# Performance work log

Measured on AMD Instinct MI355X. Metric: run time of the kernel, lower is better.

## Reference

```python
import jax, jax.numpy as jnp
import numpy as np

EPS = 1e-06
K = 4          # hc_mult
D = 2048       # hidden_size
SINKHORN_ITERS = 20


def setup_inputs() -> dict:
    key = jax.random.key(0)
    k1, k2, k3 = jax.random.split(key, 3)
    B, S = 2, 4096
    x = jax.random.normal(k1, (B, S, K, D), dtype=jnp.float32)
    out = jax.random.normal(k2, (B, S, D), dtype=jnp.float32)
    out_dim = (2 + K) * K  # 24
    # matches nn.init.normal_(std=1/sqrt(K*D))
    W = jax.random.normal(k3, (out_dim, K * D), dtype=jnp.float32) / np.sqrt(K * D)
    scale = jnp.ones((3,), dtype=jnp.float32)
    base = jnp.zeros((out_dim,), dtype=jnp.float32)
    return {"x": x, "out": out, "W": W, "scale": scale, "base": base}


def _sinkhorn(m, n_iters=SINKHORN_ITERS, eps=EPS):
    # one priming column normalization, then (n_iters-1) row/col cycles
    m = m / (jnp.sum(m, axis=-2, keepdims=True) + eps)
    for _ in range(max(n_iters - 1, 0)):
        m = m / (jnp.sum(m, axis=-1, keepdims=True) + eps)
        m = m / (jnp.sum(m, axis=-2, keepdims=True) + eps)
    return m


def reference(x, out, W, scale, base):
    out_dtype = x.dtype
    # --- _packed_logits: flatten K streams, RMS-normalize, project (fp32) ---
    flat = x.reshape(*x.shape[:-2], K * D).astype(jnp.float32)      # [B,S,K*D]
    rsqrt = jax.lax.rsqrt(jnp.mean(flat * flat, axis=-1, keepdims=True) + EPS)
    logits = jnp.einsum('bsf,of->bso', flat * rsqrt, W)             # [B,S,24]
    # --- compute_weights: split into pre/post/comb ---
    pre_logit = logits[..., :K] * scale[0] + base[:K]
    post_logit = logits[..., K:2 * K] * scale[1] + base[K:2 * K]
    comb_logit = (logits[..., 2 * K:].reshape(*logits.shape[:-1], K, K) * scale[2]
                  + base[2 * K:].reshape(K, K))
    pre = jax.nn.sigmoid(pre_logit) + EPS                           # [B,S,K]
    post = 2.0 * jax.nn.sigmoid(post_logit)                         # [B,S,K]
    comb = jax.nn.softmax(comb_logit, axis=-1) + EPS                # [B,S,K,K]
    comb = _sinkhorn(comb)                                          # doubly-stochastic
    pre = pre.astype(out_dtype)
    post = post.astype(out_dtype)
    comb = comb.astype(out_dtype)
    # --- collapse: K streams -> 1 via pre weights ---
    collapsed = jnp.sum(pre[..., None] * x, axis=-2)                # [B,S,D]
    # --- expand: write sub-block output back to K streams ---
    write = post[..., None] * out[..., None, :]                     # [B,S,K,D]
    mix = jnp.einsum('bshk,bskd->bshd', comb, x)                    # [B,S,K,D]
    y = write + mix
    return (y, collapsed)
```

## Files before the change

### kernel.cpp

```cpp
#include <hip/hip_runtime.h>


#define EPS 1e-6f
constexpr int K_ = 4, D_ = 2048, KD = 8192, NOUT = 24;
constexpr int NTOK = 2 * 4096;
constexpr int TPB = 512;
constexpr int TOKS = 3;
constexpr int NBLK = (NTOK + TOKS - 1) / TOKS;

typedef _Float16 h2 __attribute__((ext_vector_type(2)));

static __device__ __forceinline__ unsigned int pk2(float a, float b) {
    h2 h; h.x = (_Float16)a; h.y = (_Float16)b;
    return __builtin_bit_cast(unsigned int, h);
}

static __device__ __forceinline__ float dot2(unsigned int w, unsigned int x, float c) {
#if __has_builtin(__builtin_amdgcn_fdot2)
    return __builtin_amdgcn_fdot2(__builtin_bit_cast(h2, w),
                                  __builtin_bit_cast(h2, x), c, false);
#else
    h2 hw = __builtin_bit_cast(h2, w), hx = __builtin_bit_cast(h2, x);
    return c + (float)hw.x * (float)hx.x + (float)hw.y * (float)hx.y;
#endif
}

__global__ void conv_w_kernel(const float* __restrict__ W, unsigned int* __restrict__ Wh) {
    int g = blockIdx.x * blockDim.x + threadIdx.x;
    const float* src = W + (size_t)g * 8;
    float4 a = *reinterpret_cast<const float4*>(src);
    float4 b = *reinterpret_cast<const float4*>(src + 4);
    uint4 u;
    u.x = pk2(a.x, a.y); u.y = pk2(a.z, a.w);
    u.z = pk2(b.x, b.y); u.w = pk2(b.z, b.w);
    *reinterpret_cast<uint4*>(Wh + (size_t)g * 4) = u;
}

template <bool FH>
__global__ __launch_bounds__(TPB) void hypermix_kernel(
    const float* __restrict__ x, const float* __restrict__ outp,
    const unsigned int* __restrict__ Wh, const float* __restrict__ Wf,
    const float* __restrict__ scale, const float* __restrict__ base,
    float* __restrict__ y, float* __restrict__ coll)
{
    const int t = threadIdx.x;
    const int w = t >> 6, lane = t & 63;
    const size_t gt0 = (size_t)blockIdx.x * TOKS;

    __shared__ unsigned int xh[TOKS][KD / 2];
    __shared__ float ssred[TOKS][8];
    __shared__ float lg[TOKS][24];
    __shared__ float wts[TOKS][24];

#pragma unroll 1
    for (int tt = 0; tt < TOKS; ++tt) {
        float ss = 0.f;
        if (gt0 + tt < NTOK) {
            const float* xb = x + (gt0 + tt) * KD + t * 4;
#pragma unroll 2
            for (int i = 0; i < 4; ++i) {
                float4 v = *reinterpret_cast<const float4*>(xb + i * 2048);
                ss += v.x * v.x + v.y * v.y + v.z * v.z + v.w * v.w;
                uint2 p; p.x = pk2(v.x, v.y); p.y = pk2(v.z, v.w);
                *reinterpret_cast<uint2*>(&xh[tt][i * 1024 + t * 2]) = p;
            }
        }
#pragma unroll
        for (int m = 1; m < 64; m <<= 1) ss += __shfl_xor(ss, m, 64);
        if (lane == 0) ssred[tt][w] = ss;
    }
    __syncthreads();

    {
        const int r0 = w * 3;
        float acc[3][TOKS];
#pragma unroll
        for (int j = 0; j < 3; ++j)
#pragma unroll
            for (int tt = 0; tt < TOKS; ++tt) acc[j][tt] = 0.f;

#pragma unroll 2
        for (int it = 0; it < 16; ++it) {
            const int gi = it * 64 + lane;
            uint4 xv0 = *reinterpret_cast<const uint4*>(&xh[0][gi * 4]);
            uint4 xv1 = *reinterpret_cast<const uint4*>(&xh[1][gi * 4]);
            uint4 xv2 = *reinterpret_cast<const uint4*>(&xh[2][gi * 4]);
#pragma unroll
            for (int j = 0; j < 3; ++j) {
                uint4 wv;
                if (FH) {
                    wv = *reinterpret_cast<const uint4*>(
                        Wh + ((size_t)(r0 + j) * 4096 + gi * 4));
                } else {
                    const float* wr = Wf + (size_t)(r0 + j) * KD + gi * 8;
                    float4 w0 = *reinterpret_cast<const float4*>(wr);
                    float4 w1 = *reinterpret_cast<const float4*>(wr + 4);
                    wv.x = pk2(w0.x, w0.y); wv.y = pk2(w0.z, w0.w);
                    wv.z = pk2(w1.x, w1.y); wv.w = pk2(w1.z, w1.w);
                }
                acc[j][0] = dot2(wv.x, xv0.x, acc[j][0]);
                acc[j][0] = dot2(wv.y, xv0.y, acc[j][0]);
                acc[j][0] = dot2(wv.z, xv0.z, acc[j][0]);
                acc[j][0] = dot2(wv.w, xv0.w, acc[j][0]);
                acc[j][1] = dot2(wv.x, xv1.x, acc[j][1]);
                acc[j][1] = dot2(wv.y, xv1.y, acc[j][1]);
                acc[j][1] = dot2(wv.z, xv1.z, acc[j][1]);
                acc[j][1] = dot2(wv.w, xv1.w, acc[j][1]);
                acc[j][2] = dot2(wv.x, xv2.x, acc[j][2]);
                acc[j][2] = dot2(wv.y, xv2.y, acc[j][2]);
                acc[j][2] = dot2(wv.z, xv2.z, acc[j][2]);
                acc[j][2] = dot2(wv.w, xv2.w, acc[j][2]);
            }
        }
#pragma unroll
        for (int j = 0; j < 3; ++j)
#pragma unroll
            for (int tt = 0; tt < TOKS; ++tt) {
                float v = acc[j][tt];
#pragma unroll
                for (int m = 1; m < 64; m <<= 1) v += __shfl_xor(v, m, 64);
                if (lane == 0) lg[tt][r0 + j] = v;
            }
    }
    __syncthreads();

    if (t < 16 * TOKS) {
        const int wtk = t >> 4, idx = t & 15;
        float ss = 0.f;
#pragma unroll
        for (int i = 0; i < 8; ++i) ss += ssred[wtk][i];
        float rms = rsqrtf(ss * (1.f / 8192.f) + EPS);
        float s0 = scale[0], s1 = scale[1], s2 = scale[2];
        float cl = lg[wtk][8 + idx] * rms * s2 + base[8 + idx];
        float mx = fmaxf(cl, __shfl_xor(cl, 1, 64));
        mx = fmaxf(mx, __shfl_xor(mx, 2, 64));
        float e = expf(cl - mx);
        float se = e + __shfl_xor(e, 1, 64); se += __shfl_xor(se, 2, 64);
        float m = e / se + EPS;
        float cs = m + __shfl_xor(m, 4, 64); cs += __shfl_xor(cs, 8, 64);
        m = m / (cs + EPS);
#pragma unroll 1
        for (int it = 0; it < 19; ++it) {
            float rs = m + __shfl_xor(m, 1, 64); rs += __shfl_xor(rs, 2, 64);
            m = m / (rs + EPS);
            cs = m + __shfl_xor(m, 4, 64); cs += __shfl_xor(cs, 8, 64);
            m = m / (cs + EPS);
        }
        wts[wtk][8 + idx] = m;
        if (idx < 4) {
            float z = lg[wtk][idx] * rms * s0 + base[idx];
            wts[wtk][idx] = 1.f / (1.f + expf(-z)) + EPS;
        } else if (idx < 8) {
            float z = lg[wtk][idx] * rms * s1 + base[idx];
            wts[wtk][idx] = 2.f / (1.f + expf(-z));
        }
    }
    __syncthreads();

#pragma unroll 1
    for (int tt = 0; tt < TOKS; ++tt) {
        if (gt0 + tt >= NTOK) continue;
        float pre[4], post[4], cmb[4][4];
#pragma unroll
        for (int k = 0; k < 4; ++k) { pre[k] = wts[tt][k]; post[k] = wts[tt][4 + k]; }
#pragma unroll
        for (int h = 0; h < 4; ++h)
#pragma unroll
            for (int k = 0; k < 4; ++k) cmb[h][k] = wts[tt][8 + h * 4 + k];

        const int d = t * 4;
        float xk[4][4];
#pragma unroll
        for (int k = 0; k < 4; ++k) {
            uint2 p = *reinterpret_cast<const uint2*>(&xh[tt][k * 1024 + t * 2]);
            h2 h0 = __builtin_bit_cast(h2, p.x), h1 = __builtin_bit_cast(h2, p.y);
            xk[k][0] = (float)h0.x; xk[k][1] = (float)h0.y;
            xk[k][2] = (float)h1.x; xk[k][3] = (float)h1.y;
        }
        const float* ob = outp + (gt0 + tt) * D_;
        float* yb = y + (gt0 + tt) * KD;
        float* cb = coll + (gt0 + tt) * D_;
        float4 ov = *reinterpret_cast<const float4*>(ob + d);
        float cv[4], yv[4];
#pragma unroll
        for (int e = 0; e < 4; ++e)
            cv[e] = pre[0] * xk[0][e] + pre[1] * xk[1][e]
                  + pre[2] * xk[2][e] + pre[3] * xk[3][e];
        *reinterpret_cast<float4*>(cb + d) = make_float4(cv[0], cv[1], cv[2], cv[3]);
        const float oe[4] = {ov.x, ov.y, ov.z, ov.w};
#pragma unroll
        for (int h = 0; h < 4; ++h) {
#pragma unroll
            for (int e = 0; e < 4; ++e)
                yv[e] = post[h] * oe[e] + cmb[h][0] * xk[0][e] + cmb[h][1] * xk[1][e]
                      + cmb[h][2] * xk[2][e] + cmb[h][3] * xk[3][e];
            *reinterpret_cast<float4*>(yb + h * D_ + d) =
                make_float4(yv[0], yv[1], yv[2], yv[3]);
        }
    }
}

extern "C" void kernel_launch(void* const* d_in, const int* in_sizes, int n_in,
                              void* d_out, int out_size, void* d_ws, size_t ws_size,
                              hipStream_t stream) {
    const float* x     = (const float*)d_in[0];
    const float* outp  = (const float*)d_in[1];
    const float* W     = (const float*)d_in[2];
    const float* scale = (const float*)d_in[3];
    const float* base  = (const float*)d_in[4];
    float* y    = (float*)d_out;
    float* coll = y + (size_t)NTOK * KD;

    const size_t wh_bytes = (size_t)NOUT * KD * 2;
    if (ws_size >= wh_bytes) {
        unsigned int* Wh = (unsigned int*)d_ws;
        conv_w_kernel<<<NOUT * KD / 8 / 256, 256, 0, stream>>>(W, Wh);
        hypermix_kernel<true><<<NBLK, TPB, 0, stream>>>(x, outp, Wh, W, scale, base, y, coll);
    } else {
        hypermix_kernel<false><<<NBLK, TPB, 0, stream>>>(x, outp, nullptr, W, scale, base, y, coll);
    }
}
```

Measured before the change: 177.4 us.

## Batch token loads upfront, software-pipeline projection loop, serialize Sinkhorn per thread

All three tokens' x rows and out rows are loaded into registers at once, so memory loads overlap instead of running one token at a time. The GEMV loop is double-buffered by hand, issuing the next LDS and weight loads before consuming the current ones. Sinkhorn now runs in one thread per token with fast reciprocal and exp intrinsics instead of shuffles across 16 lanes. The fp32 weight fallback path is removed. The main risks are higher register pressure and a serial 3-thread tail in the Sinkhorn step.

Measured after the change: 175.5 us. Within noise of the previous version (-1.1%).

```diff
diff --git a/kernel.cpp b/kernel.cpp
--- a/kernel.cpp
+++ b/kernel.cpp
@@ -22,6 +22,14 @@
 #else
     h2 hw = __builtin_bit_cast(h2, w), hx = __builtin_bit_cast(h2, x);
     return c + (float)hw.x * (float)hx.x + (float)hw.y * (float)hx.y;
+#endif
+}
+
+static __device__ __forceinline__ float frcp(float v) {
+#if __has_builtin(__builtin_amdgcn_rcpf)
+    return __builtin_amdgcn_rcpf(v);
+#else
+    return 1.f / v;
 #endif
 }
 
@@ -36,168 +44,217 @@
     *reinterpret_cast<uint4*>(Wh + (size_t)g * 4) = u;
 }
 
-template <bool FH>
 __global__ __launch_bounds__(TPB) void hypermix_kernel(
     const float* __restrict__ x, const float* __restrict__ outp,
-    const unsigned int* __restrict__ Wh, const float* __restrict__ Wf,
+    const unsigned int* __restrict__ Wh,
     const float* __restrict__ scale, const float* __restrict__ base,
     float* __restrict__ y, float* __restrict__ coll)
 {
     const int t = threadIdx.x;
     const int w = t >> 6, lane = t & 63;
     const size_t gt0 = (size_t)blockIdx.x * TOKS;
+    const size_t tk0 = gt0;
+    const size_t tk1 = (gt0 + 1 < NTOK) ? gt0 + 1 : NTOK - 1;
+    const size_t tk2 = (gt0 + 2 < NTOK) ? gt0 + 2 : NTOK - 1;
 
     __shared__ unsigned int xh[TOKS][KD / 2];
     __shared__ float ssred[TOKS][8];
     __shared__ float lg[TOKS][24];
     __shared__ float wts[TOKS][24];
 
-#pragma unroll 1
-    for (int tt = 0; tt < TOKS; ++tt) {
-        float ss = 0.f;
-        if (gt0 + tt < NTOK) {
-            const float* xb = x + (gt0 + tt) * KD + t * 4;
-#pragma unroll 2
-            for (int i = 0; i < 4; ++i) {
-                float4 v = *reinterpret_cast<const float4*>(xb + i * 2048);
-                ss += v.x * v.x + v.y * v.y + v.z * v.z + v.w * v.w;
-                uint2 p; p.x = pk2(v.x, v.y); p.y = pk2(v.z, v.w);
-                *reinterpret_cast<uint2*>(&xh[tt][i * 1024 + t * 2]) = p;
-            }
-        }
-#pragma unroll
-        for (int m = 1; m < 64; m <<= 1) ss += __shfl_xor(ss, m, 64);
-        if (lane == 0) ssred[tt][w] = ss;
+    float4 v0[4], v1[4], v2[4], ov0, ov1, ov2;
+    {
+        const float* xb0 = x + tk0 * KD + t * 4;
+        const float* xb1 = x + tk1 * KD + t * 4;
+        const float* xb2 = x + tk2 * KD + t * 4;
+#pragma unroll
+        for (int i = 0; i < 4; ++i) v0[i] = *reinterpret_cast<const float4*>(xb0 + i * 2048);
+#pragma unroll
+        for (int i = 0; i < 4; ++i) v1[i] = *reinterpret_cast<const float4*>(xb1 + i * 2048);
+#pragma unroll
+        for (int i = 0; i < 4; ++i) v2[i] = *reinterpret_cast<const float4*>(xb2 + i * 2048);
+        ov0 = *reinterpret_cast<const float4*>(outp + tk0 * D_ + t * 4);
+        ov1 = *reinterpret_cast<const float4*>(outp + tk1 * D_ + t * 4);
+        ov2 = *reinterpret_cast<const float4*>(outp + tk2 * D_ + t * 4);
+
+        float ss0 = 0.f, ss1 = 0.f, ss2 = 0.f;
+#pragma unroll
+        for (int i = 0; i < 4; ++i) {
+            ss0 += v0[i].x * v0[i].x + v0[i].y * v0[i].y + v0[i].z * v0[i].z + v0[i].w * v0[i].w;
+            ss1 += v1[i].x * v1[i].x + v1[i].y * v1[i].y + v1[i].z * v1[i].z + v1[i].w * v1[i].w;
+            ss2 += v2[i].x * v2[i].x + v2[i].y * v2[i].y + v2[i].z * v2[i].z + v2[i].w * v2[i].w;
+            uint2 p0; p0.x = pk2(v0[i].x, v0[i].y); p0.y = pk2(v0[i].z, v0[i].w);
+            uint2 p1; p1.x = pk2(v1[i].x, v1[i].y); p1.y = pk2(v1[i].z, v1[i].w);
+            uint2 p2; p2.x = pk2(v2[i].x, v2[i].y); p2.y = pk2(v2[i].z, v2[i].w);
+            *reinterpret_cast<uint2*>(&xh[0][i * 1024 + t * 2]) = p0;
+            *reinterpret_cast<uint2*>(&xh[1][i * 1024 + t * 2]) = p1;
+            *reinterpret_cast<uint2*>(&xh[2][i * 1024 + t * 2]) = p2;
+        }
+#pragma unroll
+        for (int m = 1; m < 64; m <<= 1) {
+            ss0 += __shfl_xor(ss0, m, 64);
+            ss1 += __shfl_xor(ss1, m, 64);
+            ss2 += __shfl_xor(ss2, m, 64);
+        }
+        if (lane == 0) { ssred[0][w] = ss0; ssred[1][w] = ss1; ssred[2][w] = ss2; }
     }
     __syncthreads();
 
     {
         const int r0 = w * 3;
-        float acc[3][TOKS];
-#pragma unroll
-        for (int j = 0; j < 3; ++j)
-#pragma unroll
-            for (int tt = 0; tt < TOKS; ++tt) acc[j][tt] = 0.f;
-
-#pragma unroll 2
-        for (int it = 0; it < 16; ++it) {
-            const int gi = it * 64 + lane;
-            uint4 xv0 = *reinterpret_cast<const uint4*>(&xh[0][gi * 4]);
-            uint4 xv1 = *reinterpret_cast<const uint4*>(&xh[1][gi * 4]);
-            uint4 xv2 = *reinterpret_cast<const uint4*>(&xh[2][gi * 4]);
-#pragma unroll
-            for (int j = 0; j < 3; ++j) {
-                uint4 wv;
-                if (FH) {
-                    wv = *reinterpret_cast<const uint4*>(
-                        Wh + ((size_t)(r0 + j) * 4096 + gi * 4));
-                } else {
-                    const float* wr = Wf + (size_t)(r0 + j) * KD + gi * 8;
-                    float4 w0 = *reinterpret_cast<const float4*>(wr);
-                    float4 w1 = *reinterpret_cast<const float4*>(wr + 4);
-                    wv.x = pk2(w0.x, w0.y); wv.y = pk2(w0.z, w0.w);
-                    wv.z = pk2(w1.x, w1.y); wv.w = pk2(w1.z, w1.w);
-                }
-                acc[j][0] = dot2(wv.x, xv0.x, acc[j][0]);
-                acc[j][0] = dot2(wv.y, xv0.y, acc[j][0]);
-                acc[j][0] = dot2(wv.z, xv0.z, acc[j][0]);
-                acc[j][0] = dot2(wv.w, xv0.w, acc[j][0]);
-                acc[j][1] = dot2(wv.x, xv1.x, acc[j][1]);
-                acc[j][1] = dot2(wv.y, xv1.y, acc[j][1]);
-                acc[j][1] = dot2(wv.z, xv1.z, acc[j][1]);
-                acc[j][1] = dot2(wv.w, xv1.w, acc[j][1]);
-                acc[j][2] = dot2(wv.x, xv2.x, acc[j][2]);
-                acc[j][2] = dot2(wv.y, xv2.y, acc[j][2]);
-                acc[j][2] = dot2(wv.z, xv2.z, acc[j][2]);
-                acc[j][2] = dot2(wv.w, xv2.w, acc[j][2]);
-            }
-        }
-#pragma unroll
-        for (int j = 0; j < 3; ++j)
-#pragma unroll
-            for (int tt = 0; tt < TOKS; ++tt) {
-                float v = acc[j][tt];
-#pragma unroll
-                for (int m = 1; m < 64; m <<= 1) v += __shfl_xor(v, m, 64);
-                if (lane == 0) lg[tt][r0 + j] = v;
-            }
+        const unsigned int* Wp0 = Wh + (size_t)(r0 + 0) * 4096;
+        const unsigned int* Wp1 = Wh + (size_t)(r0 + 1) * 4096;
+        const unsigned int* Wp2 = Wh + (size_t)(r0 + 2) * 4096;
+        float a00 = 0.f, a01 = 0.f, a02 = 0.f;
+        float a10 = 0.f, a11 = 0.f, a12 = 0.f;
+        float a20 = 0.f, a21 = 0.f, a22 = 0.f;
+        uint4 xa0, xa1, xa2, wa0, wa1, wa2;
+        uint4 xb0, xb1, xb2, wb0, wb1, wb2;
+
+#define LOADIT(X0, X1, X2, W0, W1, W2, IT) do {                              \
+        const int gi4 = ((IT) * 64 + lane) * 4;                              \
+        X0 = *reinterpret_cast<const uint4*>(&xh[0][gi4]);                   \
+        X1 = *reinterpret_cast<const uint4*>(&xh[1][gi4]);                   \
+        X2 = *reinterpret_cast<const uint4*>(&xh[2][gi4]);                   \
+        W0 = *reinterpret_cast<const uint4*>(Wp0 + gi4);                     \
+        W1 = *reinterpret_cast<const uint4*>(Wp1 + gi4);                     \
+        W2 = *reinterpret_cast<const uint4*>(Wp2 + gi4);                     \
+    } while (0)
+#define DOT4(A, WV, XV) do {                                                 \
+        A = dot2(WV.x, XV.x, A); A = dot2(WV.y, XV.y, A);                    \
+        A = dot2(WV.z, XV.z, A); A = dot2(WV.w, XV.w, A);                    \
+    } while (0)
+#define CONSUME(X0, X1, X2, W0, W1, W2) do {                                 \
+        DOT4(a00, W0, X0); DOT4(a01, W0, X1); DOT4(a02, W0, X2);             \
+        DOT4(a10, W1, X0); DOT4(a11, W1, X1); DOT4(a12, W1, X2);             \
+        DOT4(a20, W2, X0); DOT4(a21, W2, X1); DOT4(a22, W2, X2);             \
+    } while (0)
+
+        LOADIT(xa0, xa1, xa2, wa0, wa1, wa2, 0);
+#pragma unroll 1
+        for (int it2 = 0; it2 < 7; ++it2) {
+            LOADIT(xb0, xb1, xb2, wb0, wb1, wb2, 2 * it2 + 1);
+            CONSUME(xa0, xa1, xa2, wa0, wa1, wa2);
+            LOADIT(xa0, xa1, xa2, wa0, wa1, wa2, 2 * it2 + 2);
+            CONSUME(xb0, xb1, xb2, wb0, wb1, wb2);
+        }
+        LOADIT(xb0, xb1, xb2, wb0, wb1, wb2, 15);
+        CONSUME(xa0, xa1, xa2, wa0, wa1, wa2);
+        CONSUME(xb0, xb1, xb2, wb0, wb1, wb2);
+#undef LOADIT
+#undef DOT4
+#undef CONSUME
+
+#pragma unroll
+        for (int m = 1; m < 64; m <<= 1) {
+            a00 += __shfl_xor(a00, m, 64); a01 += __shfl_xor(a01, m, 64);
+            a02 += __shfl_xor(a02, m, 64); a10 += __shfl_xor(a10, m, 64);
+            a11 += __shfl_xor(a11, m, 64); a12 += __shfl_xor(a12, m, 64);
+            a20 += __shfl_xor(a20, m, 64); a21 += __shfl_xor(a21, m, 64);
+            a22 += __shfl_xor(a22, m, 64);
+        }
+        if (lane == 0) {
+            lg[0][r0] = a00;     lg[1][r0] = a01;     lg[2][r0] = a02;
+            lg[0][r0 + 1] = a10; lg[1][r0 + 1] = a11; lg[2][r0 + 1] = a12;
+            lg[0][r0 + 2] = a20; lg[1][r0 + 2] = a21; lg[2][r0 + 2] = a22;
+        }
     }
     __syncthreads();
 
-    if (t < 16 * TOKS) {
-        const int wtk = t >> 4, idx = t & 15;
-        float ss = 0.f;
-#pragma unroll
-        for (int i = 0; i < 8; ++i) ss += ssred[wtk][i];
+    if (t < TOKS && gt0 + t < NTOK) {
+        float ss = ssred[t][0] + ssred[t][1] + ssred[t][2] + ssred[t][3]
+                 + ssred[t][4] + ssred[t][5] + ssred[t][6] + ssred[t][7];
         float rms = rsqrtf(ss * (1.f / 8192.f) + EPS);
         float s0 = scale[0], s1 = scale[1], s2 = scale[2];
-        float cl = lg[wtk][8 + idx] * rms * s2 + base[8 + idx];
-        float mx = fmaxf(cl, __shfl_xor(cl, 1, 64));
-        mx = fmaxf(mx, __shfl_xor(mx, 2, 64));
-        float e = expf(cl - mx);
-        float se = e + __shfl_xor(e, 1, 64); se += __shfl_xor(se, 2, 64);
-        float m = e / se + EPS;
-        float cs = m + __shfl_xor(m, 4, 64); cs += __shfl_xor(cs, 8, 64);
-        m = m / (cs + EPS);
+        float l[24];
+#pragma unroll
+        for (int i = 0; i < 24; ++i) l[i] = lg[t][i];
+#pragma unroll
+        for (int k = 0; k < 4; ++k) {
+            float z0 = l[k] * rms * s0 + base[k];
+            wts[t][k] = frcp(1.f + __expf(-z0)) + EPS;
+            float z1 = l[4 + k] * rms * s1 + base[4 + k];
+            wts[t][4 + k] = 2.f * frcp(1.f + __expf(-z1));
+        }
+        float p[16];
+#pragma unroll
+        for (int h = 0; h < 4; ++h) {
+            float c0 = l[8 + h * 4 + 0] * rms * s2 + base[8 + h * 4 + 0];
+            float c1 = l[8 + h * 4 + 1] * rms * s2 + base[8 + h * 4 + 1];
+            float c2 = l[8 + h * 4 + 2] * rms * s2 + base[8 + h * 4 + 2];
+            float c3 = l[8 + h * 4 + 3] * rms * s2 + base[8 + h * 4 + 3];
+            float mx = fmaxf(fmaxf(c0, c1), fmaxf(c2, c3));
+            float e0 = __expf(c0 - mx), e1 = __expf(c1 - mx);
+            float e2 = __expf(c2 - mx), e3 = __expf(c3 - mx);
+            float inv = frcp(e0 + e1 + e2 + e3);
+            p[h * 4 + 0] = e0 * inv + EPS; p[h * 4 + 1] = e1 * inv + EPS;
+            p[h * 4 + 2] = e2 * inv + EPS; p[h * 4 + 3] = e3 * inv + EPS;
+        }
+#pragma unroll
+        for (int k = 0; k < 4; ++k) {
+            float inv = frcp(p[k] + p[4 + k] + p[8 + k] + p[12 + k] + EPS);
+            p[k] *= inv; p[4 + k] *= inv; p[8 + k] *= inv; p[12 + k] *= inv;
+        }
 #pragma unroll 1
-        for (int it = 0; it < 19; ++it) {
-            float rs = m + __shfl_xor(m, 1, 64); rs += __shfl_xor(rs, 2, 64);
-            m = m / (rs + EPS);
-            cs = m + __shfl_xor(m, 4, 64); cs += __shfl_xor(cs, 8, 64);
-            m = m / (cs + EPS);
-        }
-        wts[wtk][8 + idx] = m;
-        if (idx < 4) {
-            float z = lg[wtk][idx] * rms * s0 + base[idx];
-            wts[wtk][idx] = 1.f / (1.f + expf(-z)) + EPS;
-        } else if (idx < 8) {
-            float z = lg[wtk][idx] * rms * s1 + base[idx];
-            wts[wtk][idx] = 2.f / (1.f + expf(-z));
-        }
+        for (int itn = 0; itn < 19; ++itn) {
+#pragma unroll
+            for (int h = 0; h < 4; ++h) {
+                float inv = frcp(p[h * 4] + p[h * 4 + 1] + p[h * 4 + 2] + p[h * 4 + 3] + EPS);
+                p[h * 4] *= inv; p[h * 4 + 1] *= inv; p[h * 4 + 2] *= inv; p[h * 4 + 3] *= inv;
+            }
+#pragma unroll
+            for (int k = 0; k < 4; ++k) {
+                float inv = frcp(p[k] + p[4 + k] + p[8 + k] + p[12 + k] + EPS);
+                p[k] *= inv; p[4 + k] *= inv; p[8 + k] *= inv; p[12 + k] *= inv;
+            }
+        }
+#pragma unroll
+        for (int i = 0; i < 16; ++i) wts[t][8 + i] = p[i];
     }
     __syncthreads();
 
-#pragma unroll 1
-    for (int tt = 0; tt < TOKS; ++tt) {
-        if (gt0 + tt >= NTOK) continue;
-        float pre[4], post[4], cmb[4][4];
-#pragma unroll
-        for (int k = 0; k < 4; ++k) { pre[k] = wts[tt][k]; post[k] = wts[tt][4 + k]; }
-#pragma unroll
-        for (int h = 0; h < 4; ++h)
-#pragma unroll
-            for (int k = 0; k < 4; ++k) cmb[h][k] = wts[tt][8 + h * 4 + k];
-
-        const int d = t * 4;
-        float xk[4][4];
-#pragma unroll
-        for (int k = 0; k < 4; ++k) {
-            uint2 p = *reinterpret_cast<const uint2*>(&xh[tt][k * 1024 + t * 2]);
-            h2 h0 = __builtin_bit_cast(h2, p.x), h1 = __builtin_bit_cast(h2, p.y);
-            xk[k][0] = (float)h0.x; xk[k][1] = (float)h0.y;
-            xk[k][2] = (float)h1.x; xk[k][3] = (float)h1.y;
-        }
-        const float* ob = outp + (gt0 + tt) * D_;
-        float* yb = y + (gt0 + tt) * KD;
-        float* cb = coll + (gt0 + tt) * D_;
-        float4 ov = *reinterpret_cast<const float4*>(ob + d);
-        float cv[4], yv[4];
-#pragma unroll
-        for (int e = 0; e < 4; ++e)
-            cv[e] = pre[0] * xk[0][e] + pre[1] * xk[1][e]
-                  + pre[2] * xk[2][e] + pre[3] * xk[3][e];
-        *reinterpret_cast<float4*>(cb + d) = make_float4(cv[0], cv[1], cv[2], cv[3]);
-        const float oe[4] = {ov.x, ov.y, ov.z, ov.w};
-#pragma unroll
-        for (int h = 0; h < 4; ++h) {
-#pragma unroll
-            for (int e = 0; e < 4; ++e)
-                yv[e] = post[h] * oe[e] + cmb[h][0] * xk[0][e] + cmb[h][1] * xk[1][e]
-                      + cmb[h][2] * xk[2][e] + cmb[h][3] * xk[3][e];
-            *reinterpret_cast<float4*>(yb + h * D_ + d) =
-                make_float4(yv[0], yv[1], yv[2], yv[3]);
-        }
-    }
+#define PHASEB(TT, OV) do {                                                  \
+    if (gt0 + TT < NTOK) {                                                   \
+        float pre[4], post[4], cmb[4][4];                                    \
+        _Pragma("unroll")                                                    \
+        for (int k = 0; k < 4; ++k) { pre[k] = wts[TT][k]; post[k] = wts[TT][4 + k]; } \
+        _Pragma("unroll")                                                    \
+        for (int h = 0; h < 4; ++h)                                          \
+            _Pragma("unroll")                                                \
+            for (int k = 0; k < 4; ++k) cmb[h][k] = wts[TT][8 + h * 4 + k];  \
+        const int d = t * 4;                                                 \
+        float xk[4][4];                                                      \
+        _Pragma("unroll")                                                    \
+        for (int k = 0; k < 4; ++k) {                                        \
+            uint2 pq = *reinterpret_cast<const uint2*>(&xh[TT][k * 1024 + t * 2]); \
+            h2 h0 = __builtin_bit_cast(h2, pq.x), h1 = __builtin_bit_cast(h2, pq.y); \
+            xk[k][0] = (float)h0.x; xk[k][1] = (float)h0.y;                  \
+            xk[k][2] = (float)h1.x; xk[k][3] = (float)h1.y;                  \
+        }                                                                    \
+        float* yb = y + (gt0 + TT) * KD;                                     \
+        float* cb = coll + (gt0 + TT) * D_;                                  \
+        float cv[4], yv[4];                                                  \
+        _Pragma("unroll")                                                    \
+        for (int e = 0; e < 4; ++e)                                          \
+            cv[e] = pre[0] * xk[0][e] + pre[1] * xk[1][e]                    \
+                  + pre[2] * xk[2][e] + pre[3] * xk[3][e];                   \
+        *reinterpret_cast<float4*>(cb + d) = make_float4(cv[0], cv[1], cv[2], cv[3]); \
+        const float oe[4] = {OV.x, OV.y, OV.z, OV.w};                        \
+        _Pragma("unroll")                                                    \
+        for (int h = 0; h < 4; ++h) {                                        \
+            _Pragma("unroll")                                                \
+            for (int e = 0; e < 4; ++e)                                      \
+                yv[e] = post[h] * oe[e] + cmb[h][0] * xk[0][e] + cmb[h][1] * xk[1][e] \
+                      + cmb[h][2] * xk[2][e] + cmb[h][3] * xk[3][e];         \
+            *reinterpret_cast<float4*>(yb + h * D_ + d) =                    \
+                make_float4(yv[0], yv[1], yv[2], yv[3]);                     \
+        }                                                                    \
+    } } while (0)
+
+    PHASEB(0, ov0);
+    PHASEB(1, ov1);
+    PHASEB(2, ov2);
+#undef PHASEB
 }
 
 extern "C" void kernel_launch(void* const* d_in, const int* in_sizes, int n_in,
@@ -211,12 +268,7 @@
     float* y    = (float*)d_out;
     float* coll = y + (size_t)NTOK * KD;
 
-    const size_t wh_bytes = (size_t)NOUT * KD * 2;
-    if (ws_size >= wh_bytes) {
-        unsigned int* Wh = (unsigned int*)d_ws;
-        conv_w_kernel<<<NOUT * KD / 8 / 256, 256, 0, stream>>>(W, Wh);
-        hypermix_kernel<true><<<NBLK, TPB, 0, stream>>>(x, outp, Wh, W, scale, base, y, coll);
-    } else {
-        hypermix_kernel<false><<<NBLK, TPB, 0, stream>>>(x, outp, nullptr, W, scale, base, y, coll);
-    }
-}
+    unsigned int* Wh = (unsigned int*)d_ws;
+    conv_w_kernel<<<NOUT * KD / 8 / 256, 256, 0, stream>>>(W, Wh);
+    hypermix_kernel<<<NBLK, TPB, 0, stream>>>(x, outp, Wh, scale, base, y, coll);
+}
```

## Process four tokens per block with software-pipelined projection and per-thread sinkhorn

Applied to the files above, without the earlier changes.

Raises tokens per block from 3 to 4 so each fp16 weight load feeds four token dot products, and software-pipelines the projection loop with double-buffered register loads of x and W. The out tensor is prefetched during the initial x load. Sinkhorn and the gates are computed by one thread per token with fast exp and reciprocal instead of shuffles across 16 lanes. Also adds a launch bound of 2 blocks per SM and drops the fp32-weight fallback. Risks: more shared memory and registers per block, and less parallel work in the serial sinkhorn phase.

After: 195.6 us. 10.3% more time.

```diff
diff --git a/kernel.cpp b/kernel.cpp
--- a/kernel.cpp
+++ b/kernel.cpp
@@ -5,8 +5,8 @@
 constexpr int K_ = 4, D_ = 2048, KD = 8192, NOUT = 24;
 constexpr int NTOK = 2 * 4096;
 constexpr int TPB = 512;
-constexpr int TOKS = 3;
-constexpr int NBLK = (NTOK + TOKS - 1) / TOKS;
+constexpr int TOKS = 4;
+constexpr int NBLK = NTOK / TOKS;
 
 typedef _Float16 h2 __attribute__((ext_vector_type(2)));
 
@@ -22,6 +22,14 @@
 #else
     h2 hw = __builtin_bit_cast(h2, w), hx = __builtin_bit_cast(h2, x);
     return c + (float)hw.x * (float)hx.x + (float)hw.y * (float)hx.y;
+#endif
+}
+
+static __device__ __forceinline__ float frcp(float v) {
+#if __has_builtin(__builtin_amdgcn_rcpf)
+    return __builtin_amdgcn_rcpf(v);
+#else
+    return 1.f / v;
 #endif
 }
 
@@ -36,10 +44,9 @@
     *reinterpret_cast<uint4*>(Wh + (size_t)g * 4) = u;
 }
 
-template <bool FH>
-__global__ __launch_bounds__(TPB) void hypermix_kernel(
+__global__ __launch_bounds__(TPB, 2) void hypermix_kernel(
     const float* __restrict__ x, const float* __restrict__ outp,
-    const unsigned int* __restrict__ Wh, const float* __restrict__ Wf,
+    const unsigned int* __restrict__ Wh,
     const float* __restrict__ scale, const float* __restrict__ base,
     float* __restrict__ y, float* __restrict__ coll)
 {
@@ -52,18 +59,21 @@
     __shared__ float lg[TOKS][24];
     __shared__ float wts[TOKS][24];
 
-#pragma unroll 1
+    float4 ovr[4];
+#pragma unroll 2
     for (int tt = 0; tt < TOKS; ++tt) {
+        const float* xb = x + (gt0 + tt) * KD + t * 4;
+        float4 v[4];
+#pragma unroll
+        for (int i = 0; i < 4; ++i)
+            v[i] = *reinterpret_cast<const float4*>(xb + i * 2048);
+        ovr[tt] = *reinterpret_cast<const float4*>(outp + (gt0 + tt) * D_ + t * 4);
         float ss = 0.f;
-        if (gt0 + tt < NTOK) {
-            const float* xb = x + (gt0 + tt) * KD + t * 4;
-#pragma unroll 2
-            for (int i = 0; i < 4; ++i) {
-                float4 v = *reinterpret_cast<const float4*>(xb + i * 2048);
-                ss += v.x * v.x + v.y * v.y + v.z * v.z + v.w * v.w;
-                uint2 p; p.x = pk2(v.x, v.y); p.y = pk2(v.z, v.w);
-                *reinterpret_cast<uint2*>(&xh[tt][i * 1024 + t * 2]) = p;
-            }
+#pragma unroll
+        for (int i = 0; i < 4; ++i) {
+            ss += v[i].x * v[i].x + v[i].y * v[i].y + v[i].z * v[i].z + v[i].w * v[i].w;
+            uint2 p; p.x = pk2(v[i].x, v[i].y); p.y = pk2(v[i].z, v[i].w);
+            *reinterpret_cast<uint2*>(&xh[tt][i * 1024 + t * 2]) = p;
         }
 #pragma unroll
         for (int m = 1; m < 64; m <<= 1) ss += __shfl_xor(ss, m, 64);
@@ -73,49 +83,60 @@
 
     {
         const int r0 = w * 3;
-        float acc[3][TOKS];
+        const unsigned int* Wp0 = Wh + (size_t)(r0 + 0) * 4096;
+        const unsigned int* Wp1 = Wh + (size_t)(r0 + 1) * 4096;
+        const unsigned int* Wp2 = Wh + (size_t)(r0 + 2) * 4096;
+        float acc[3][4];
 #pragma unroll
         for (int j = 0; j < 3; ++j)
 #pragma unroll
-            for (int tt = 0; tt < TOKS; ++tt) acc[j][tt] = 0.f;
-
-#pragma unroll 2
-        for (int it = 0; it < 16; ++it) {
-            const int gi = it * 64 + lane;
-            uint4 xv0 = *reinterpret_cast<const uint4*>(&xh[0][gi * 4]);
-            uint4 xv1 = *reinterpret_cast<const uint4*>(&xh[1][gi * 4]);
-            uint4 xv2 = *reinterpret_cast<const uint4*>(&xh[2][gi * 4]);
-#pragma unroll
-            for (int j = 0; j < 3; ++j) {
-                uint4 wv;
-                if (FH) {
-                    wv = *reinterpret_cast<const uint4*>(
-                        Wh + ((size_t)(r0 + j) * 4096 + gi * 4));
-                } else {
-                    const float* wr = Wf + (size_t)(r0 + j) * KD + gi * 8;
-                    float4 w0 = *reinterpret_cast<const float4*>(wr);
-                    float4 w1 = *reinterpret_cast<const float4*>(wr + 4);
-                    wv.x = pk2(w0.x, w0.y); wv.y = pk2(w0.z, w0.w);
-                    wv.z = pk2(w1.x, w1.y); wv.w = pk2(w1.z, w1.w);
-                }
-                acc[j][0] = dot2(wv.x, xv0.x, acc[j][0]);
-                acc[j][0] = dot2(wv.y, xv0.y, acc[j][0]);
-                acc[j][0] = dot2(wv.z, xv0.z, acc[j][0]);
-                acc[j][0] = dot2(wv.w, xv0.w, acc[j][0]);
-                acc[j][1] = dot2(wv.x, xv1.x, acc[j][1]);
-                acc[j][1] = dot2(wv.y, xv1.y, acc[j][1]);
-                acc[j][1] = dot2(wv.z, xv1.z, acc[j][1]);
-                acc[j][1] = dot2(wv.w, xv1.w, acc[j][1]);
-                acc[j][2] = dot2(wv.x, xv2.x, acc[j][2]);
-                acc[j][2] = dot2(wv.y, xv2.y, acc[j][2]);
-                acc[j][2] = dot2(wv.z, xv2.z, acc[j][2]);
-                acc[j][2] = dot2(wv.w, xv2.w, acc[j][2]);
-            }
-        }
+            for (int tt = 0; tt < 4; ++tt) acc[j][tt] = 0.f;
+
+        uint4 xa0, xa1, xa2, xa3, wa0, wa1, wa2;
+        uint4 xb0, xb1, xb2, xb3, wb0, wb1, wb2;
+
+#define LOADIT(X0, X1, X2, X3, W0, W1, W2, IT) do {                          \
+        const int gi4 = ((IT) * 64 + lane) * 4;                              \
+        X0 = *reinterpret_cast<const uint4*>(&xh[0][gi4]);                   \
+        X1 = *reinterpret_cast<const uint4*>(&xh[1][gi4]);                   \
+        X2 = *reinterpret_cast<const uint4*>(&xh[2][gi4]);                   \
+        X3 = *reinterpret_cast<const uint4*>(&xh[3][gi4]);                   \
+        W0 = *reinterpret_cast<const uint4*>(Wp0 + gi4);                     \
+        W1 = *reinterpret_cast<const uint4*>(Wp1 + gi4);                     \
+        W2 = *reinterpret_cast<const uint4*>(Wp2 + gi4);                     \
+    } while (0)
+#define DOT4(A, WV, XV) do {                                                 \
+        A = dot2(WV.x, XV.x, A); A = dot2(WV.y, XV.y, A);                    \
+        A = dot2(WV.z, XV.z, A); A = dot2(WV.w, XV.w, A);                    \
+    } while (0)
+#define CONSUME(X0, X1, X2, X3, W0, W1, W2) do {                             \
+        DOT4(acc[0][0], W0, X0); DOT4(acc[0][1], W0, X1);                    \
+        DOT4(acc[0][2], W0, X2); DOT4(acc[0][3], W0, X3);                    \
+        DOT4(acc[1][0], W1, X0); DOT4(acc[1][1], W1, X1);                    \
+        DOT4(acc[1][2], W1, X2); DOT4(acc[1][3], W1, X3);                    \
+        DOT4(acc[2][0], W2, X0); DOT4(acc[2][1], W2, X1);                    \
+        DOT4(acc[2][2], W2, X2); DOT4(acc[2][3], W2, X3);                    \
+    } while (0)
+
+        LOADIT(xa0, xa1, xa2, xa3, wa0, wa1, wa2, 0);
+#pragma unroll 1
+        for (int it2 = 0; it2 < 7; ++it2) {
+            LOADIT(xb0, xb1, xb2, xb3, wb0, wb1, wb2, 2 * it2 + 1);
+            CONSUME(xa0, xa1, xa2, xa3, wa0, wa1, wa2);
+            LOADIT(xa0, xa1, xa2, xa3, wa0, wa1, wa2, 2 * it2 + 2);
+            CONSUME(xb0, xb1, xb2, xb3, wb0, wb1, wb2);
+        }
+        LOADIT(xb0, xb1, xb2, xb3, wb0, wb1, wb2, 15);
+        CONSUME(xa0, xa1, xa2, xa3, wa0, wa1, wa2);
+        CONSUME(xb0, xb1, xb2, xb3, wb0, wb1, wb2);
+#undef LOADIT
+#undef DOT4
+#undef CONSUME
+
 #pragma unroll
         for (int j = 0; j < 3; ++j)
 #pragma unroll
-            for (int tt = 0; tt < TOKS; ++tt) {
+            for (int tt = 0; tt < 4; ++tt) {
                 float v = acc[j][tt];
 #pragma unroll
                 for (int m = 1; m < 64; m <<= 1) v += __shfl_xor(v, m, 64);
@@ -124,42 +145,60 @@
     }
     __syncthreads();
 
-    if (t < 16 * TOKS) {
-        const int wtk = t >> 4, idx = t & 15;
-        float ss = 0.f;
-#pragma unroll
-        for (int i = 0; i < 8; ++i) ss += ssred[wtk][i];
+    if (t < TOKS) {
+        float ss = ssred[t][0] + ssred[t][1] + ssred[t][2] + ssred[t][3]
+                 + ssred[t][4] + ssred[t][5] + ssred[t][6] + ssred[t][7];
         float rms = rsqrtf(ss * (1.f / 8192.f) + EPS);
         float s0 = scale[0], s1 = scale[1], s2 = scale[2];
-        float cl = lg[wtk][8 + idx] * rms * s2 + base[8 + idx];
-        float mx = fmaxf(cl, __shfl_xor(cl, 1, 64));
-        mx = fmaxf(mx, __shfl_xor(mx, 2, 64));
-        float e = expf(cl - mx);
-        float se = e + __shfl_xor(e, 1, 64); se += __shfl_xor(se, 2, 64);
-        float m = e / se + EPS;
-        float cs = m + __shfl_xor(m, 4, 64); cs += __shfl_xor(cs, 8, 64);
-        m = m / (cs + EPS);
+        float l[24];
+#pragma unroll
+        for (int i = 0; i < 24; ++i) l[i] = lg[t][i];
+#pragma unroll
+        for (int k = 0; k < 4; ++k) {
+            float z0 = l[k] * rms * s0 + base[k];
+            wts[t][k] = frcp(1.f + __expf(-z0)) + EPS;
+            float z1 = l[4 + k] * rms * s1 + base[4 + k];
+            wts[t][4 + k] = 2.f * frcp(1.f + __expf(-z1));
+        }
+        float p[16];
+#pragma unroll
+        for (int h = 0; h < 4; ++h) {
+            float c0 = l[8 + h * 4 + 0] * rms * s2 + base[8 + h * 4 + 0];
+            float c1 = l[8 + h * 4 + 1] * rms * s2 + base[8 + h * 4 + 1];
+            float c2 = l[8 + h * 4 + 2] * rms * s2 + base[8 + h * 4 + 2];
+            float c3 = l[8 + h * 4 + 3] * rms * s2 + base[8 + h * 4 + 3];
+            float mx = fmaxf(fmaxf(c0, c1), fmaxf(c2, c3));
+            float e0 = __expf(c0 - mx), e1 = __expf(c1 - mx);
+            float e2 = __expf(c2 - mx), e3 = __expf(c3 - mx);
+            float inv = frcp(e0 + e1 + e2 + e3);
+            p[h * 4 + 0] = e0 * inv + EPS; p[h * 4 + 1] = e1 * inv + EPS;
+            p[h * 4 + 2] = e2 * inv + EPS; p[h * 4 + 3] = e3 * inv + EPS;
+        }
+#pragma unroll
+        for (int k = 0; k < 4; ++k) {
+            float inv = frcp(p[k] + p[4 + k] + p[8 + k] + p[12 + k] + EPS);
+            p[k] *= inv; p[4 + k] *= inv; p[8 + k] *= inv; p[12 + k] *= inv;
+        }
 #pragma unroll 1
-        for (int it = 0; it < 19; ++it) {
-            float rs = m + __shfl_xor(m, 1, 64); rs += __shfl_xor(rs, 2, 64);
-            m = m / (rs + EPS);
-            cs = m + __shfl_xor(m, 4, 64); cs += __shfl_xor(cs, 8, 64);
-            m = m / (cs + EPS);
-        }
-        wts[wtk][8 + idx] = m;
-        if (idx < 4) {
-            float z = lg[wtk][idx] * rms * s0 + base[idx];
-            wts[wtk][idx] = 1.f / (1.f + expf(-z)) + EPS;
-        } else if (idx < 8) {
-            float z = lg[wtk][idx] * rms * s1 + base[idx];
-            wts[wtk][idx] = 2.f / (1.f + expf(-z));
-        }
+        for (int itn = 0; itn < 19; ++itn) {
+#pragma unroll
+            for (int h = 0; h < 4; ++h) {
+                float inv = frcp(p[h * 4] + p[h * 4 + 1] + p[h * 4 + 2] + p[h * 4 + 3] + EPS);
+                p[h * 4] *= inv; p[h * 4 + 1] *= inv; p[h * 4 + 2] *= inv; p[h * 4 + 3] *= inv;
+            }
+#pragma unroll
+            for (int k = 0; k < 4; ++k) {
+                float inv = frcp(p[k] + p[4 + k] + p[8 + k] + p[12 + k] + EPS);
+                p[k] *= inv; p[4 + k] *= inv; p[8 + k] *= inv; p[12 + k] *= inv;
+            }
+        }
+#pragma unroll
+        for (int i = 0; i < 16; ++i) wts[t][8 + i] = p[i];
     }
     __syncthreads();
 
 #pragma unroll 1
     for (int tt = 0; tt < TOKS; ++tt) {
-        if (gt0 + tt >= NTOK) continue;
         float pre[4], post[4], cmb[4][4];
 #pragma unroll
         for (int k = 0; k < 4; ++k) { pre[k] = wts[tt][k]; post[k] = wts[tt][4 + k]; }
@@ -172,22 +211,20 @@
         float xk[4][4];
 #pragma unroll
         for (int k = 0; k < 4; ++k) {
-            uint2 p = *reinterpret_cast<const uint2*>(&xh[tt][k * 1024 + t * 2]);
-            h2 h0 = __builtin_bit_cast(h2, p.x), h1 = __builtin_bit_cast(h2, p.y);
+            uint2 pq = *reinterpret_cast<const uint2*>(&xh[tt][k * 1024 + t * 2]);
+            h2 h0 = __builtin_bit_cast(h2, pq.x), h1 = __builtin_bit_cast(h2, pq.y);
             xk[k][0] = (float)h0.x; xk[k][1] = (float)h0.y;
             xk[k][2] = (float)h1.x; xk[k][3] = (float)h1.y;
         }
-        const float* ob = outp + (gt0 + tt) * D_;
         float* yb = y + (gt0 + tt) * KD;
         float* cb = coll + (gt0 + tt) * D_;
-        float4 ov = *reinterpret_cast<const float4*>(ob + d);
         float cv[4], yv[4];
 #pragma unroll
         for (int e = 0; e < 4; ++e)
             cv[e] = pre[0] * xk[0][e] + pre[1] * xk[1][e]
                   + pre[2] * xk[2][e] + pre[3] * xk[3][e];
         *reinterpret_cast<float4*>(cb + d) = make_float4(cv[0], cv[1], cv[2], cv[3]);
-        const float oe[4] = {ov.x, ov.y, ov.z, ov.w};
+        const float oe[4] = {ovr[tt].x, ovr[tt].y, ovr[tt].z, ovr[tt].w};
 #pragma unroll
         for (int h = 0; h < 4; ++h) {
 #pragma unroll
@@ -211,12 +248,7 @@
     float* y    = (float*)d_out;
     float* coll = y + (size_t)NTOK * KD;
 
-    const size_t wh_bytes = (size_t)NOUT * KD * 2;
-    if (ws_size >= wh_bytes) {
-        unsigned int* Wh = (unsigned int*)d_ws;
-        conv_w_kernel<<<NOUT * KD / 8 / 256, 256, 0, stream>>>(W, Wh);
-        hypermix_kernel<true><<<NBLK, TPB, 0, stream>>>(x, outp, Wh, W, scale, base, y, coll);
-    } else {
-        hypermix_kernel<false><<<NBLK, TPB, 0, stream>>>(x, outp, nullptr, W, scale, base, y, coll);
-    }
-}
+    unsigned int* Wh = (unsigned int*)d_ws;
+    conv_w_kernel<<<NOUT * KD / 8 / 256, 256, 0, stream>>>(W, Wh);
+    hypermix_kernel<<<NBLK, TPB, 0, stream>>>(x, outp, Wh, scale, base, y, coll);
+}
```
